# Kernel optimization log

Measured on AMD Instinct MI355X. Metric: run time of the kernel, lower is better.

## Reference

```python
import jax, jax.numpy as jnp
import numpy as np

NEG_SLOPE = 0.2  # PyG GATv2Conv default negative_slope


def gatv2_conv(x, src, dst, n_nodes, Wl, bl, Wr, br, att, bias):
    """One GATv2Conv layer (concat=True, add_self_loops already applied).
    x: [N, Fin]; src/dst: [E]; Wl/Wr: [Fin, H*C]; att: [H, C]; bias: [H*C].
    Returns [N, H*C]."""
    H, C = att.shape
    xl = (x @ Wl + bl).reshape(n_nodes, H, C)  # source transform (x_j)
    xr = (x @ Wr + br).reshape(n_nodes, H, C)  # target transform (x_i)
    # per-edge GATv2 score: a^T LeakyReLU(xl_j + xr_i)
    e = jax.nn.leaky_relu(xl[src] + xr[dst], NEG_SLOPE)      # [E, H, C]
    score = jnp.einsum('ehc,hc->eh', e, att)                 # [E, H]
    # segment softmax over incoming edges of each destination node
    m = jax.lax.stop_gradient(
        jax.ops.segment_max(score, dst, num_segments=n_nodes))  # [N, H]
    p = jnp.exp(score - m[dst])                               # [E, H]
    s = jax.ops.segment_sum(p, dst, num_segments=n_nodes)     # [N, H]
    alpha = p / s[dst]                                        # [E, H]
    out = jax.ops.segment_sum(alpha[:, :, None] * xl[src], dst,
                              num_segments=n_nodes)           # [N, H, C]
    return out.reshape(n_nodes, H * C) + bias


def setup_inputs() -> dict:
    key = jax.random.key(0)
    ks = jax.random.split(key, 16)
    N, Fin, H, C = 20000, 64, 4, 64
    E = 500000
    Fmid = H * C  # 256

    def glorot(k, shape):
        fan_in, fan_out = shape[0], shape[-1]
        lim = np.sqrt(6.0 / (fan_in + fan_out))
        return jax.random.uniform(k, shape, jnp.float32, -lim, lim)

    return {
        'x': jax.random.normal(ks[0], (N, Fin), jnp.float32),
        'edge_index': jax.random.randint(ks[1], (2, E), 0, N, jnp.int64),
        # layer 1: in=64, out=64, heads=4
        'Wl1': glorot(ks[2], (Fin, H * C)),
        'bl1': jnp.zeros((H * C,), jnp.float32),
        'Wr1': glorot(ks[3], (Fin, H * C)),
        'br1': jnp.zeros((H * C,), jnp.float32),
        'att1': glorot(ks[4], (H, C)),
        'bias1': jnp.zeros((H * C,), jnp.float32),
        # layer 2: in=256, out=64, heads=4
        'Wl2': glorot(ks[5], (Fmid, H * C)),
        'bl2': jnp.zeros((H * C,), jnp.float32),
        'Wr2': glorot(ks[6], (Fmid, H * C)),
        'br2': jnp.zeros((H * C,), jnp.float32),
        'att2': glorot(ks[7], (H, C)),
        'bias2': jnp.zeros((H * C,), jnp.float32),
    }


def reference(x, edge_index, Wl1, bl1, Wr1, br1, att1, bias1,
              Wl2, bl2, Wr2, br2, att2, bias2):
    N = x.shape[0]
    # PyG add_self_loops=True default
    loop = jnp.arange(N, dtype=edge_index.dtype)
    src = jnp.concatenate([edge_index[0], loop])
    dst = jnp.concatenate([edge_index[1], loop])

    h = gatv2_conv(x, src, dst, N, Wl1, bl1, Wr1, br1, att1, bias1)
    h = jax.nn.elu(h)
    h = gatv2_conv(h, src, dst, N, Wl2, bl2, Wr2, br2, att2, bias2)
    return (h, jax.nn.log_softmax(h, axis=1))
```

## Files before the change

### kernel.cpp

```cpp
#include <hip/hip_runtime.h>
#include <math.h>

#define NEG_SLOPE 0.2f

typedef unsigned short ushort_t;
typedef __attribute__((ext_vector_type(8))) short short8;
typedef __attribute__((ext_vector_type(4))) float float4v;
typedef _Float16 half2v __attribute__((ext_vector_type(2)));

#if defined(__has_builtin)
#if __has_builtin(__builtin_amdgcn_fdot2)
#define HAS_FDOT2 1
#endif
#endif

__device__ __forceinline__ ushort_t f2bf(float f) {
    unsigned u = __float_as_uint(f);
    return (ushort_t)((u + 0x7fffu + ((u >> 16) & 1u)) >> 16);
}
__device__ __forceinline__ unsigned pack2bf(float lo, float hi) {
    return ((unsigned)f2bf(hi) << 16) | (unsigned)f2bf(lo);
}

__global__ void hist_kernel(const int* __restrict__ dst, int* __restrict__ deg, int E) {
    int i = blockIdx.x * 256 + threadIdx.x;
    if (i < E) atomicAdd(&deg[dst[i]], 1);
}

__global__ void partial_kernel(const int* __restrict__ deg, int* __restrict__ partial, int n) {
    const int t = threadIdx.x;
    const int i = blockIdx.x * 256 + t;
    int v = (i < n) ? deg[i] : 0;
#pragma unroll
    for (int off = 32; off > 0; off >>= 1) v += __shfl_xor(v, off, 64);
    __shared__ int ws[4];
    if ((t & 63) == 0) ws[t >> 6] = v;
    __syncthreads();
    if (t == 0) partial[blockIdx.x] = ws[0] + ws[1] + ws[2] + ws[3];
}

__global__ void scan_kernel(const int* __restrict__ in, int* __restrict__ out, int n) {
    __shared__ int sm[1024];
    __shared__ int carry_s;
    const int t = threadIdx.x;
    if (t == 0) { carry_s = 0; out[0] = 0; }
    __syncthreads();
    for (int base = 0; base < n; base += 1024) {
        int v = (base + t < n) ? in[base + t] : 0;
        sm[t] = v;
        __syncthreads();
        for (int off = 1; off < 1024; off <<= 1) {
            int u = (t >= off) ? sm[t - off] : 0;
            __syncthreads();
            sm[t] += u;
            __syncthreads();
        }
        if (base + t < n) out[base + t + 1] = carry_s + sm[t];
        __syncthreads();
        if (t == 0) carry_s += sm[1023];
        __syncthreads();
    }
}

__global__ void scan_block_kernel(const int* __restrict__ deg, const int* __restrict__ blk_off,
                                  int* __restrict__ row_ptr, int n) {
    const int t = threadIdx.x;
    const int i = blockIdx.x * 256 + t;
    const int lane = t & 63, w = t >> 6;
    int x = (i < n) ? deg[i] : 0;
#pragma unroll
    for (int off = 1; off < 64; off <<= 1) {
        int u = __shfl_up(x, off, 64);
        if (lane >= off) x += u;
    }
    __shared__ int ws[4];
    if (lane == 63) ws[w] = x;
    __syncthreads();
    int add = blk_off[blockIdx.x];
#pragma unroll
    for (int j = 0; j < 4; ++j)
        if (j < w) add += ws[j];
    if (i < n) row_ptr[i + 1] = add + x;
    if (i == 0) row_ptr[0] = 0;
}

__global__ void scatter_kernel(const int* __restrict__ src, const int* __restrict__ dst,
                               const int* __restrict__ row_ptr, int* __restrict__ cursor,
                               int* __restrict__ csr_src, int E) {
    int i = blockIdx.x * 256 + threadIdx.x;
    if (i < E) {
        int d = dst[i];
        int pos = row_ptr[d] + atomicAdd(&cursor[d], 1);
        csr_src[pos] = src[i];
    }
}

__global__ void wt_all_kernel(const float* __restrict__ W1l, const float* __restrict__ W1r,
                              const float* __restrict__ W2l, const float* __restrict__ W2r,
                              ushort_t* __restrict__ T1l, ushort_t* __restrict__ T1r,
                              ushort_t* __restrict__ T2l, ushort_t* __restrict__ T2r) {
    const int b = blockIdx.x;
    const float* W;
    ushort_t* T;
    int K, idx;
    if (b < 64)       { W = W1l; T = T1l; K = 64;  idx = b * 256 + threadIdx.x; }
    else if (b < 128) { W = W1r; T = T1r; K = 64;  idx = (b - 64) * 256 + threadIdx.x; }
    else if (b < 384) { W = W2l; T = T2l; K = 256; idx = (b - 128) * 256 + threadIdx.x; }
    else              { W = W2r; T = T2r; K = 256; idx = (b - 384) * 256 + threadIdx.x; }
    const int k = idx >> 8, c = idx & 255;
    T[(size_t)c * K + k] = f2bf(W[idx]);
}

template <int K, bool A_FP32>
__global__ __launch_bounds__(256) void gemm_dual_kernel(const void* __restrict__ Av,
                                                        const ushort_t* __restrict__ BTl,
                                                        const ushort_t* __restrict__ BTr,
                                                        const float* __restrict__ bl,
                                                        const float* __restrict__ br,
                                                        _Float16* __restrict__ outl,
                                                        _Float16* __restrict__ outr, int M) {
    __shared__ ushort_t As[2][64][40];
    __shared__ ushort_t Bs[2][2][128][40];
    const int t = threadIdx.x;
    const int row0 = blockIdx.x * 64, col0 = blockIdx.y * 128;
    const int wid = t >> 6, lane = t & 63;
    const int wr = wid >> 1, wc = wid & 1;
    const int frow = lane & 15, fk = (lane >> 4) * 8;
    const int arow = t >> 2, ak8 = (t & 3) * 8;
    const int srow = t >> 1, sks = (t & 1) * 16;

    float4v acc[2][2][4];
#pragma unroll
    for (int m = 0; m < 2; ++m)
#pragma unroll
        for (int i = 0; i < 2; ++i)
#pragma unroll
            for (int j = 0; j < 4; ++j) acc[m][i][j] = (float4v){0.f, 0.f, 0.f, 0.f};

    auto stage = [&](int buf, int k0) {
        uint4 va = make_uint4(0, 0, 0, 0);
        if (row0 + arow < M) {
            if (A_FP32) {
                const float* Xf = (const float*)Av + (size_t)(row0 + arow) * K + k0 + ak8;
                float4 x0 = *(const float4*)(Xf + 0);
                float4 x1 = *(const float4*)(Xf + 4);
                va = make_uint4(pack2bf(x0.x, x0.y), pack2bf(x0.z, x0.w),
                                pack2bf(x1.x, x1.y), pack2bf(x1.z, x1.w));
            } else {
                va = *(const uint4*)((const ushort_t*)Av + (size_t)(row0 + arow) * K + k0 + ak8);
            }
        }
        *(uint4*)&As[buf][arow][ak8] = va;
        const ushort_t* Bp = BTl + (size_t)(col0 + srow) * K + k0 + sks;
        *(uint4*)&Bs[buf][0][srow][sks + 0] = *(const uint4*)(Bp + 0);
        *(uint4*)&Bs[buf][0][srow][sks + 8] = *(const uint4*)(Bp + 8);
        const ushort_t* Bq = BTr + (size_t)(col0 + srow) * K + k0 + sks;
        *(uint4*)&Bs[buf][1][srow][sks + 0] = *(const uint4*)(Bq + 0);
        *(uint4*)&Bs[buf][1][srow][sks + 8] = *(const uint4*)(Bq + 8);
    };

    stage(0, 0);
    __syncthreads();
    int cur = 0;
    for (int k0 = 0; k0 < K; k0 += 32) {
        if (k0 + 32 < K) stage(cur ^ 1, k0 + 32);
        short8 af[2], bf[2][4];
#pragma unroll
        for (int mi = 0; mi < 2; ++mi)
            af[mi] = *(const short8*)&As[cur][wr * 32 + mi * 16 + frow][fk];
#pragma unroll
        for (int m = 0; m < 2; ++m)
#pragma unroll
            for (int ni = 0; ni < 4; ++ni)
                bf[m][ni] = *(const short8*)&Bs[cur][m][wc * 64 + ni * 16 + frow][fk];
#pragma unroll
        for (int m = 0; m < 2; ++m)
#pragma unroll
            for (int mi = 0; mi < 2; ++mi)
#pragma unroll
                for (int ni = 0; ni < 4; ++ni)
                    acc[m][mi][ni] = __builtin_amdgcn_mfma_f32_16x16x32_bf16(
                        af[mi], bf[m][ni], acc[m][mi][ni], 0, 0, 0);
        __syncthreads();
        cur ^= 1;
    }

    const int crow = (lane >> 4) * 4;
#pragma unroll
    for (int ni = 0; ni < 4; ++ni) {
        const int col = col0 + wc * 64 + ni * 16 + frow;
        const float bvl = bl[col], bvr = br[col];
#pragma unroll
        for (int mi = 0; mi < 2; ++mi) {
#pragma unroll
            for (int r = 0; r < 4; ++r) {
                const int row = row0 + wr * 32 + mi * 16 + crow + r;
                if (row < M) {
                    outl[(size_t)row * 256 + col] = (_Float16)(acc[0][mi][ni][r] + bvl);
                    outr[(size_t)row * 256 + col] = (_Float16)(acc[1][mi][ni][r] + bvr);
                }
            }
        }
    }
}

__global__ __launch_bounds__(256) void gat_fused_kernel(const int* __restrict__ csr_src,
                                                        const int* __restrict__ row_ptr,
                                                        const _Float16* __restrict__ xl,
                                                        const _Float16* __restrict__ xr,
                                                        const float* __restrict__ att,
                                                        const float* __restrict__ bias,
                                                        ushort_t* __restrict__ out_b,
                                                        float* __restrict__ out,
                                                        float* __restrict__ out_ls,
                                                        int n_nodes, int apply_elu) {
    const int wv = threadIdx.x >> 6;
    const int d = blockIdx.x * 4 + wv;
    if (d >= n_nodes) return;
    const int lane = threadIdx.x & 63;
    const int e = lane >> 5;
    const int g = lane & 31;
    const int off = g * 8;

    union U8 { uint4 u; _Float16 h[8]; half2v h2[4]; };
    U8 xru;
    xru.u = *(const uint4*)(xr + (size_t)d * 256 + off);
    float avf[8];
    *(float4*)&avf[0] = *(const float4*)(att + off);
    *(float4*)&avf[4] = *(const float4*)(att + off + 4);
#if HAS_FDOT2
    half2v xr2[4], a06[4], a04[4];
#pragma unroll
    for (int i = 0; i < 4; ++i) {
        xr2[i] = xru.h2[i];
        a06[i] = (half2v){(_Float16)(0.6f * avf[2 * i]), (_Float16)(0.6f * avf[2 * i + 1])};
        a04[i] = (half2v){(_Float16)(0.4f * avf[2 * i]), (_Float16)(0.4f * avf[2 * i + 1])};
    }
#else
    float xrf[8];
#pragma unroll
    for (int i = 0; i < 8; ++i) xrf[i] = (float)xru.h[i];
#endif
    const int e0 = row_ptr[d];
    const int deg = row_ptr[d + 1] - e0;
    const int cnt = deg + 1;
    const int nchunk = (cnt + 1) >> 1;
    float m = -INFINITY, s_loc = 0.f;
    float acc8[8] = {0.f, 0.f, 0.f, 0.f, 0.f, 0.f, 0.f, 0.f};

    U8 gc, g1;
    {
        const int j = e;
        const int sn = (j < deg) ? csr_src[e0 + j] : d;
        gc.u = *(const uint4*)(xl + (size_t)sn * 256 + off);
    }
    g1.u = make_uint4(0, 0, 0, 0);
    if (nchunk > 1) {
        const int j = 2 + e;
        const int sn = (j < deg) ? csr_src[e0 + j] : d;
        g1.u = *(const uint4*)(xl + (size_t)sn * 256 + off);
    }
    int sn_nxt = d;
    if (nchunk > 2) {
        const int j = 4 + e;
        sn_nxt = (j < deg) ? csr_src[e0 + j] : d;
    }

    for (int c = 0; c < nchunk; ++c) {
        const int base = c << 1;
        int sn_n3 = d;
        if (c + 3 < nchunk) {
            const int j = base + 6 + e;
            sn_n3 = (j < deg) ? csr_src[e0 + j] : d;
        }
        U8 g2;
        g2.u = make_uint4(0, 0, 0, 0);
        if (c + 2 < nchunk) g2.u = *(const uint4*)(xl + (size_t)sn_nxt * 256 + off);

        const int j = base + e;
        float sc = 0.f;
#if HAS_FDOT2
#pragma unroll
        for (int i = 0; i < 4; ++i) {
            half2v v = gc.h2[i] + xr2[i];
            unsigned vb = __builtin_bit_cast(unsigned, v);
            half2v va = __builtin_bit_cast(half2v, vb & 0x7fff7fffu);
            sc = __builtin_amdgcn_fdot2(v, a06[i], sc, false);
            sc = __builtin_amdgcn_fdot2(va, a04[i], sc, false);
        }
#else
#pragma unroll
        for (int i = 0; i < 8; ++i) {
            float v = (float)gc.h[i] + xrf[i];
            v = fmaxf(v, NEG_SLOPE * v);
            sc = fmaf(v, avf[i], sc);
        }
#endif
        sc += __shfl_xor(sc, 1, 64);
        sc += __shfl_xor(sc, 2, 64);
        sc += __shfl_xor(sc, 4, 64);
        sc = (j < cnt) ? sc : -INFINITY;
        float mx = fmaxf(sc, __shfl_xor(sc, 32, 64));
        if (mx > m + 8.f) {
            const float g2f = __expf(m - mx);
            s_loc *= g2f;
#pragma unroll
            for (int i = 0; i < 8; ++i) acc8[i] *= g2f;
            m = mx;
        }
        const float p = __expf(sc - m);
        s_loc += p;
#pragma unroll
        for (int i = 0; i < 8; ++i)
            acc8[i] = fmaf(p, (float)gc.h[i], acc8[i]);

        gc = g1;
        g1 = g2;
        sn_nxt = sn_n3;
    }

    float s_tot = s_loc + __shfl_xor(s_loc, 32, 64);
#pragma unroll
    for (int i = 0; i < 8; ++i) acc8[i] += __shfl_xor(acc8[i], 32, 64);
    const float inv_s = 1.f / s_tot;
    float o8[8];
    const float* bp = bias + off;
#pragma unroll
    for (int i = 0; i < 8; ++i) o8[i] = acc8[i] * inv_s + bp[i];

    if (apply_elu) {
#pragma unroll
        for (int i = 0; i < 8; ++i) o8[i] = o8[i] > 0.f ? o8[i] : (__expf(o8[i]) - 1.f);
        if (e == 0) {
            uint4 u;
            u.x = pack2bf(o8[0], o8[1]);
            u.y = pack2bf(o8[2], o8[3]);
            u.z = pack2bf(o8[4], o8[5]);
            u.w = pack2bf(o8[6], o8[7]);
            *(uint4*)(out_b + (size_t)d * 256 + off) = u;
        }
    } else {
        if (e == 0) {
            float* op = out + (size_t)d * 256 + off;
            *(float4*)op       = make_float4(o8[0], o8[1], o8[2], o8[3]);
            *(float4*)(op + 4) = make_float4(o8[4], o8[5], o8[6], o8[7]);
        }
        float mx = o8[0];
#pragma unroll
        for (int i = 1; i < 8; ++i) mx = fmaxf(mx, o8[i]);
        mx = fmaxf(mx, __shfl_xor(mx, 1, 64));
        mx = fmaxf(mx, __shfl_xor(mx, 2, 64));
        mx = fmaxf(mx, __shfl_xor(mx, 4, 64));
        mx = fmaxf(mx, __shfl_xor(mx, 8, 64));
        mx = fmaxf(mx, __shfl_xor(mx, 16, 64));
        float se = 0.f;
#pragma unroll
        for (int i = 0; i < 8; ++i) se += __expf(o8[i] - mx);
        se += __shfl_xor(se, 1, 64);
        se += __shfl_xor(se, 2, 64);
        se += __shfl_xor(se, 4, 64);
        se += __shfl_xor(se, 8, 64);
        se += __shfl_xor(se, 16, 64);
        const float lg = mx + __logf(se);
        if (e == 0) {
            float* lp = out_ls + (size_t)d * 256 + off;
            *(float4*)lp       = make_float4(o8[0] - lg, o8[1] - lg, o8[2] - lg, o8[3] - lg);
            *(float4*)(lp + 4) = make_float4(o8[4] - lg, o8[5] - lg, o8[6] - lg, o8[7] - lg);
        }
    }
}

extern "C" void kernel_launch(void* const* d_in, const int* in_sizes, int n_in,
                              void* d_out, int out_size, void* d_ws, size_t ws_size,
                              hipStream_t stream) {
    const float* x     = (const float*)d_in[0];
    const int*   edge  = (const int*)d_in[1];
    const float* Wl1   = (const float*)d_in[2];
    const float* bl1   = (const float*)d_in[3];
    const float* Wr1   = (const float*)d_in[4];
    const float* br1   = (const float*)d_in[5];
    const float* att1  = (const float*)d_in[6];
    const float* bias1 = (const float*)d_in[7];
    const float* Wl2   = (const float*)d_in[8];
    const float* bl2   = (const float*)d_in[9];
    const float* Wr2   = (const float*)d_in[10];
    const float* br2   = (const float*)d_in[11];
    const float* att2  = (const float*)d_in[12];
    const float* bias2 = (const float*)d_in[13];

    const int N = in_sizes[0] / 64;
    const int E = in_sizes[1] / 2;
    const int* srcI = edge;
    const int* dstI = edge + E;

    const size_t NM = (size_t)N * 256;
    _Float16*  XR   = (_Float16*)d_ws;
    ushort_t*  XB   = (ushort_t*)(XR + NM);
    _Float16*  XL   = (_Float16*)(XB + NM);
    ushort_t*  WT1l = (ushort_t*)(XL + NM);
    ushort_t*  WT1r = WT1l + 256 * 64;
    ushort_t*  WT2l = WT1r + 256 * 64;
    ushort_t*  WT2r = WT2l + 256 * 256;
    int* deg     = (int*)(WT2r + 256 * 256);
    int* row_ptr = deg + N;
    int* cursor  = row_ptr + N + 1;
    int* partial = cursor + N;
    int* blk_off = partial + ((N + 255) / 256);
    int* csr_src = blk_off + ((N + 255) / 256) + 1;

    const int nb = (N + 255) / 256;
    const int e_grid = (E + 255) / 256;
    const dim3 gemm_grid((N + 63) / 64, 2);
    const int gat_grid = (N + 3) / 4;

    wt_all_kernel<<<640, 256, 0, stream>>>(Wl1, Wr1, Wl2, Wr2, WT1l, WT1r, WT2l, WT2r);

    hipMemsetAsync(deg, 0, (size_t)N * sizeof(int), stream);
    hipMemsetAsync(cursor, 0, (size_t)N * sizeof(int), stream);
    hist_kernel<<<e_grid, 256, 0, stream>>>(dstI, deg, E);
    partial_kernel<<<nb, 256, 0, stream>>>(deg, partial, N);
    scan_kernel<<<1, 1024, 0, stream>>>(partial, blk_off, nb);
    scan_block_kernel<<<nb, 256, 0, stream>>>(deg, blk_off, row_ptr, N);
    scatter_kernel<<<e_grid, 256, 0, stream>>>(srcI, dstI, row_ptr, cursor, csr_src, E);

    gemm_dual_kernel<64, true><<<gemm_grid, 256, 0, stream>>>(x, WT1l, WT1r, bl1, br1,
                                                              XL, XR, N);
    gat_fused_kernel<<<gat_grid, 256, 0, stream>>>(csr_src, row_ptr, XL, XR, att1, bias1,
                                                   XB, nullptr, nullptr, N, 1);

    gemm_dual_kernel<256, false><<<gemm_grid, 256, 0, stream>>>(XB, WT2l, WT2r, bl2, br2,
                                                                XL, XR, N);
    float* h2 = (float*)d_out;
    gat_fused_kernel<<<gat_grid, 256, 0, stream>>>(csr_src, row_ptr, XL, XR, att2, bias2,
                                                   nullptr, h2, h2 + NM, N, 0);
}
```

Baseline: 216.0 us.

## Process destination nodes in descending-degree order and shorten gather prefetch depth

Adds a counting sort of destination nodes by in-degree (histogram, scan, scatter kernels) and has the GAT aggregation kernel read each wave's node from that order. High-degree nodes are scheduled first, which aims to reduce tail imbalance across waves. The gather pipeline is also cut from two chunks of lookahead to one, lowering register use per wave at the cost of less latency hiding. The sort adds three small kernel launches and two memsets per call, and destination nodes are now written in scattered order.

```diff
diff --git a/kernel.cpp b/kernel.cpp
--- a/kernel.cpp
+++ b/kernel.cpp
@@ -92,6 +92,41 @@
         int d = dst[i];
         int pos = row_ptr[d] + atomicAdd(&cursor[d], 1);
         csr_src[pos] = src[i];
+    }
+}
+
+__global__ void dhist_kernel(const int* __restrict__ row_ptr, int* __restrict__ dhist, int n) {
+    int i = blockIdx.x * 256 + threadIdx.x;
+    if (i < n) {
+        int dg = row_ptr[i + 1] - row_ptr[i];
+        int b = 511 - min(dg, 511);
+        atomicAdd(&dhist[b], 1);
+    }
+}
+
+__global__ void dscan_kernel(const int* __restrict__ dhist, int* __restrict__ doff) {
+    __shared__ int sm[512];
+    const int t = threadIdx.x;
+    const int v = dhist[t];
+    sm[t] = v;
+    __syncthreads();
+    for (int off = 1; off < 512; off <<= 1) {
+        int u = (t >= off) ? sm[t - off] : 0;
+        __syncthreads();
+        sm[t] += u;
+        __syncthreads();
+    }
+    doff[t] = sm[t] - v;
+}
+
+__global__ void dscatter_kernel(const int* __restrict__ row_ptr, const int* __restrict__ doff,
+                                int* __restrict__ dcursor, int* __restrict__ order, int n) {
+    int i = blockIdx.x * 256 + threadIdx.x;
+    if (i < n) {
+        int dg = row_ptr[i + 1] - row_ptr[i];
+        int b = 511 - min(dg, 511);
+        int pos = doff[b] + atomicAdd(&dcursor[b], 1);
+        order[pos] = i;
     }
 }
 
@@ -204,7 +239,8 @@
     }
 }
 
-__global__ __launch_bounds__(256) void gat_fused_kernel(const int* __restrict__ csr_src,
+__global__ __launch_bounds__(256) void gat_fused_kernel(const int* __restrict__ order,
+                                                        const int* __restrict__ csr_src,
                                                         const int* __restrict__ row_ptr,
                                                         const _Float16* __restrict__ xl,
                                                         const _Float16* __restrict__ xr,
@@ -215,8 +251,9 @@
                                                         float* __restrict__ out_ls,
                                                         int n_nodes, int apply_elu) {
     const int wv = threadIdx.x >> 6;
-    const int d = blockIdx.x * 4 + wv;
-    if (d >= n_nodes) return;
+    const int gi = blockIdx.x * 4 + wv;
+    if (gi >= n_nodes) return;
+    const int d = order[gi];
     const int lane = threadIdx.x & 63;
     const int e = lane >> 5;
     const int g = lane & 31;
@@ -248,34 +285,28 @@
     float m = -INFINITY, s_loc = 0.f;
     float acc8[8] = {0.f, 0.f, 0.f, 0.f, 0.f, 0.f, 0.f, 0.f};
 
-    U8 gc, g1;
+    U8 gc;
     {
         const int j = e;
         const int sn = (j < deg) ? csr_src[e0 + j] : d;
         gc.u = *(const uint4*)(xl + (size_t)sn * 256 + off);
     }
-    g1.u = make_uint4(0, 0, 0, 0);
+    int sn_nxt = d;
     if (nchunk > 1) {
         const int j = 2 + e;
-        const int sn = (j < deg) ? csr_src[e0 + j] : d;
-        g1.u = *(const uint4*)(xl + (size_t)sn * 256 + off);
-    }
-    int sn_nxt = d;
-    if (nchunk > 2) {
-        const int j = 4 + e;
         sn_nxt = (j < deg) ? csr_src[e0 + j] : d;
     }
 
     for (int c = 0; c < nchunk; ++c) {
         const int base = c << 1;
-        int sn_n3 = d;
-        if (c + 3 < nchunk) {
-            const int j = base + 6 + e;
-            sn_n3 = (j < deg) ? csr_src[e0 + j] : d;
-        }
-        U8 g2;
-        g2.u = make_uint4(0, 0, 0, 0);
-        if (c + 2 < nchunk) g2.u = *(const uint4*)(xl + (size_t)sn_nxt * 256 + off);
+        int sn_n2 = d;
+        if (c + 2 < nchunk) {
+            const int j = base + 4 + e;
+            sn_n2 = (j < deg) ? csr_src[e0 + j] : d;
+        }
+        U8 gn;
+        gn.u = make_uint4(0, 0, 0, 0);
+        if (c + 1 < nchunk) gn.u = *(const uint4*)(xl + (size_t)sn_nxt * 256 + off);
 
         const int j = base + e;
         float sc = 0.f;
@@ -314,9 +345,8 @@
         for (int i = 0; i < 8; ++i)
             acc8[i] = fmaf(p, (float)gc.h[i], acc8[i]);
 
-        gc = g1;
-        g1 = g2;
-        sn_nxt = sn_n3;
+        gc = gn;
+        sn_nxt = sn_n2;
     }
 
     float s_tot = s_loc + __shfl_xor(s_loc, 32, 64);
@@ -406,7 +436,11 @@
     int* cursor  = row_ptr + N + 1;
     int* partial = cursor + N;
     int* blk_off = partial + ((N + 255) / 256);
-    int* csr_src = blk_off + ((N + 255) / 256) + 1;
+    int* order   = blk_off + ((N + 255) / 256) + 1;
+    int* dhist   = order + N;
+    int* doff    = dhist + 512;
+    int* dcursor = doff + 512;
+    int* csr_src = dcursor + 512;
 
     const int nb = (N + 255) / 256;
     const int e_grid = (E + 255) / 256;
@@ -417,20 +451,25 @@
 
     hipMemsetAsync(deg, 0, (size_t)N * sizeof(int), stream);
     hipMemsetAsync(cursor, 0, (size_t)N * sizeof(int), stream);
+    hipMemsetAsync(dhist, 0, 512 * sizeof(int), stream);
+    hipMemsetAsync(dcursor, 0, 512 * sizeof(int), stream);
     hist_kernel<<<e_grid, 256, 0, stream>>>(dstI, deg, E);
     partial_kernel<<<nb, 256, 0, stream>>>(deg, partial, N);
     scan_kernel<<<1, 1024, 0, stream>>>(partial, blk_off, nb);
     scan_block_kernel<<<nb, 256, 0, stream>>>(deg, blk_off, row_ptr, N);
     scatter_kernel<<<e_grid, 256, 0, stream>>>(srcI, dstI, row_ptr, cursor, csr_src, E);
+    dhist_kernel<<<nb, 256, 0, stream>>>(row_ptr, dhist, N);
+    dscan_kernel<<<1, 512, 0, stream>>>(dhist, doff);
+    dscatter_kernel<<<nb, 256, 0, stream>>>(row_ptr, doff, dcursor, order, N);
 
     gemm_dual_kernel<64, true><<<gemm_grid, 256, 0, stream>>>(x, WT1l, WT1r, bl1, br1,
                                                               XL, XR, N);
-    gat_fused_kernel<<<gat_grid, 256, 0, stream>>>(csr_src, row_ptr, XL, XR, att1, bias1,
-                                                   XB, nullptr, nullptr, N, 1);
+    gat_fused_kernel<<<gat_grid, 256, 0, stream>>>(order, csr_src, row_ptr, XL, XR,
+                                                   att1, bias1, XB, nullptr, nullptr, N, 1);
 
     gemm_dual_kernel<256, false><<<gemm_grid, 256, 0, stream>>>(XB, WT2l, WT2r, bl2, br2,
                                                                 XL, XR, N);
     float* h2 = (float*)d_out;
-    gat_fused_kernel<<<gat_grid, 256, 0, stream>>>(csr_src, row_ptr, XL, XR, att2, bias2,
-                                                   nullptr, h2, h2 + NM, N, 0);
-}
+    gat_fused_kernel<<<gat_grid, 256, 0, stream>>>(order, csr_src, row_ptr, XL, XR,
+                                                   att2, bias2, nullptr, h2, h2 + NM, N, 0);
+}
```

New measurement: 311.4 us. +44.2%, slower.
